# Performance work log

Measured on AMD Instinct MI355X. Metric: run time of the kernel, lower is better.

## Reference

```python
import jax, jax.numpy as jnp
import numpy as np

EMBED_DIM = 1024
NUM_HEADS = 16
HEAD_DIM = EMBED_DIM // NUM_HEADS


def setup_inputs() -> dict:
    key = jax.random.key(0)
    ks = jax.random.split(key, 9)
    B, S, D = 4, 2048, EMBED_DIM
    s = 1.0 / np.sqrt(D)
    return {
        "x": jax.random.normal(ks[0], (B, S, D), dtype=jnp.float32),
        "Wq": jax.random.normal(ks[1], (D, D), dtype=jnp.float32) * s,
        "bq": jnp.zeros((D,), dtype=jnp.float32),
        "Wk": jax.random.normal(ks[2], (D, D), dtype=jnp.float32) * s,
        "bk": jnp.zeros((D,), dtype=jnp.float32),
        "Wv": jax.random.normal(ks[3], (D, D), dtype=jnp.float32) * s,
        "bv": jnp.zeros((D,), dtype=jnp.float32),
        "Wo": jax.random.normal(ks[4], (D, D), dtype=jnp.float32) * s,
        "bo": jnp.zeros((D,), dtype=jnp.float32),
    }


def reference(x, Wq, bq, Wk, bk, Wv, bv, Wo, bo):
    B, S, D = x.shape
    H, Hd = NUM_HEADS, HEAD_DIM

    def proj(W, b):
        # [B,S,D] -> [B,H,S,Hd]
        y = jnp.einsum('bsd,de->bse', x, W) + b
        return y.reshape(B, S, H, Hd).transpose(0, 2, 1, 3)

    q = proj(Wq, bq)
    k = proj(Wk, bk)
    v = proj(Wv, bv)

    scale = 1.0 / jnp.sqrt(jnp.asarray(Hd, dtype=x.dtype))
    scores = jnp.einsum('bhqd,bhkd->bhqk', q, k) * scale  # [B,H,S,S]
    attn = jax.nn.softmax(scores, axis=-1)
    # dropout is identity in eval/inference mode
    heads = jnp.einsum('bhqk,bhkd->bhqd', attn, v)  # [B,H,S,Hd]
    heads = heads.transpose(0, 2, 1, 3).reshape(B, S, D)
    z = jnp.einsum('bsd,de->bse', heads, Wo) + bo
    return z
```

## Files before the change

### kernel.cpp

```cpp
#include <hip/hip_runtime.h>


typedef __attribute__((ext_vector_type(8))) short bf16x8;
typedef __attribute__((ext_vector_type(4))) float f32x4;
typedef __attribute__((ext_vector_type(4))) unsigned int u32x4;

#define MFMA16 __builtin_amdgcn_mfma_f32_16x16x32_bf16

__device__ __forceinline__ unsigned short f2bf(float f) {
  unsigned int u = __float_as_uint(f);
  u += 0x7fff + ((u >> 16) & 1);
  return (unsigned short)(u >> 16);
}

__device__ __forceinline__ unsigned int pkbf(float lo, float hi) {
  unsigned int a = __float_as_uint(lo) + 0x8000u;
  unsigned int b = __float_as_uint(hi) + 0x8000u;
  return __builtin_amdgcn_perm(b, a, 0x07060302u);
}

__device__ __forceinline__ bf16x8 pack4(unsigned int a, unsigned int b,
                                        unsigned int c, unsigned int d) {
  union { u32x4 u; bf16x8 v; } t;
  t.u = (u32x4){a, b, c, d};
  return t.v;
}

__device__ __forceinline__ void gl2l16(const unsigned short* g, unsigned short* l) {
  __builtin_amdgcn_global_load_lds((const __attribute__((address_space(1))) void*)g,
                                   (__attribute__((address_space(3))) void*)l, 16, 0, 0);
}
__device__ __forceinline__ void gl2l4(const unsigned short* g, unsigned short* l) {
  __builtin_amdgcn_global_load_lds((const __attribute__((address_space(1))) void*)g,
                                   (__attribute__((address_space(3))) void*)l, 4, 0, 0);
}

__global__ __launch_bounds__(256) void k_prep(const float* __restrict__ x,
                                              unsigned short* __restrict__ xb,
                                              const float* w0, const float* w1,
                                              const float* w2, const float* w3,
                                              unsigned short* o0, unsigned short* o1,
                                              unsigned short* o2, unsigned short* o3) {
  const int bid = blockIdx.x, tid = threadIdx.x;
  if (bid < 8192) {
    int i = (bid * 256 + tid) * 4;
    float4 v = *(const float4*)(x + i);
    ushort4 u;
    u.x = f2bf(v.x); u.y = f2bf(v.y); u.z = f2bf(v.z); u.w = f2bf(v.w);
    *(ushort4*)(xb + i) = u;
  } else {
    __shared__ float t[32][33];
    int tt = bid - 8192;
    int z = tt >> 10, rem = tt & 1023;
    const float* W = z == 0 ? w0 : z == 1 ? w1 : z == 2 ? w2 : w3;
    unsigned short* O = z == 0 ? o0 : z == 1 ? o1 : z == 2 ? o2 : o3;
    int e0 = (rem & 31) * 32, d0 = (rem >> 5) * 32;
    int tx = tid & 31, ty = tid >> 5;
    #pragma unroll
    for (int i = 0; i < 4; i++)
      t[ty + i * 8][tx] = W[(d0 + ty + i * 8) * 1024 + e0 + tx];
    __syncthreads();
    #pragma unroll
    for (int i = 0; i < 4; i++)
      O[(e0 + ty + i * 8) * 1024 + d0 + tx] = f2bf(t[tx][ty + i * 8]);
  }
}

__device__ __forceinline__ void kloop64(const unsigned short* __restrict__ gA,
                                        const unsigned short* __restrict__ gB,
                                        unsigned short* As, unsigned short* Bs,
                                        int w, int fm, int quad, int wr, int wc,
                                        f32x4 (&acc)[4][4]) {
  const int fsw = fm & 7;
  const int cs0 = (quad ^ fsw) * 8;
  const int cs1 = ((quad + 4) ^ fsw) * 8;
  unsigned short* lA = As + w * 2048;
  unsigned short* lB = Bs + w * 2048;

  for (int kb = 0; kb < 1024; kb += 64) {
    __syncthreads();
    #pragma unroll
    for (int i = 0; i < 4; i++) {
      gl2l16(gA + kb + i * 8192, lA + i * 512);
      gl2l16(gB + kb + i * 8192, lB + i * 512);
    }
    __syncthreads();
    #pragma unroll
    for (int kh = 0; kh < 2; kh++) {
      const int cs = kh ? cs1 : cs0;
      bf16x8 af[4], bfr[4];
      #pragma unroll
      for (int mt = 0; mt < 4; mt++)
        af[mt] = *(const bf16x8*)&As[(wr + mt * 16 + fm) * 64 + cs];
      #pragma unroll
      for (int nt = 0; nt < 4; nt++)
        bfr[nt] = *(const bf16x8*)&Bs[(wc + nt * 16 + fm) * 64 + cs];
      #pragma unroll
      for (int mt = 0; mt < 4; mt++)
        #pragma unroll
        for (int nt = 0; nt < 4; nt++)
          acc[mt][nt] = MFMA16(af[mt], bfr[nt], acc[mt][nt], 0, 0, 0);
    }
  }
}

__global__ __launch_bounds__(256) void gemm_qkv(const unsigned short* __restrict__ A,
                                                const unsigned short* __restrict__ Wt,
                                                const float* __restrict__ biq,
                                                const float* __restrict__ bik,
                                                const float* __restrict__ biv,
                                                unsigned short* __restrict__ oq,
                                                unsigned short* __restrict__ ok,
                                                unsigned short* __restrict__ ov,
                                                float qscale) {
  const int bid = blockIdx.x;
  const int xcd = bid & 7, c = bid >> 3;
  const int by = c & 63;
  const int phase = c >> 6;
  const int bx = xcd + phase * 8;
  const int bm0 = by * 128;
  const int bn0g = bx * 128;
  const int z = phase, bn0 = bn0g & 1023;

  const float* bias = z == 0 ? biq : z == 1 ? bik : biv;
  unsigned short* out = z == 0 ? oq : z == 1 ? ok : ov;
  const float scale = z == 0 ? qscale : 1.0f;

  const int tid = threadIdx.x;
  const int lane = tid & 63, w = tid >> 6;
  const int wr = (w >> 1) * 64, wc = (w & 1) * 64;
  const int fm = lane & 15, quad = lane >> 4;

  __shared__ unsigned short As[128 * 64];
  __shared__ unsigned short Bs[128 * 64];

  f32x4 acc[4][4] = {};

  const int srow = lane >> 3;
  const int sswz = ((lane & 7) ^ srow) * 8;
  const unsigned short* gA = A + (size_t)(bm0 + w * 32 + srow) * 1024 + sswz;
  const unsigned short* gB = Wt + (size_t)(bn0g + w * 32 + srow) * 1024 + sswz;

  kloop64(gA, gB, As, Bs, w, fm, quad, wr, wc, acc);

  float bv[4];
  #pragma unroll
  for (int nt = 0; nt < 4; nt++) bv[nt] = bias[bn0 + wc + nt * 16 + fm];

  #pragma unroll
  for (int mt = 0; mt < 4; mt++) {
    #pragma unroll
    for (int nt = 0; nt < 4; nt++) {
      #pragma unroll
      for (int r = 0; r < 4; r++) {
        int row = bm0 + wr + mt * 16 + quad * 4 + r;
        int col = bn0 + wc + nt * 16 + fm;
        float v = (acc[mt][nt][r] + bv[nt]) * scale;
        int b = row >> 11, s = row & 2047, h = col >> 6, hd = col & 63;
        if (z < 2)
          out[(((b << 4) + h) * 2048 + s) * 64 + hd] = f2bf(v);
        else
          out[(((b << 4) + h) * 64 + hd) * 2048 + s] = f2bf(v);
      }
    }
  }
}

__global__ __launch_bounds__(256) void gemm_out(const unsigned short* __restrict__ A,
                                                const unsigned short* __restrict__ Bt,
                                                const float* __restrict__ bias,
                                                float* __restrict__ out) {
  const int bid = blockIdx.x;
  const int xcd = bid & 7, c = bid >> 3;
  const int by = xcd * 8 + (c >> 3);
  const int bx = c & 7;
  const int bm0 = by * 128, bn0 = bx * 128;

  const int tid = threadIdx.x;
  const int lane = tid & 63, w = tid >> 6;
  const int wr = (w >> 1) * 64, wc = (w & 1) * 64;
  const int fm = lane & 15, quad = lane >> 4;

  __shared__ unsigned short As[128 * 64];
  __shared__ unsigned short Bs[128 * 64];

  f32x4 acc[4][4] = {};

  const int srow = lane >> 3;
  const int sswz = ((lane & 7) ^ srow) * 8;
  const unsigned short* gA = A + (size_t)(bm0 + w * 32 + srow) * 1024 + sswz;
  const unsigned short* gB = Bt + (size_t)(bn0 + w * 32 + srow) * 1024 + sswz;

  kloop64(gA, gB, As, Bs, w, fm, quad, wr, wc, acc);

  float bv[4];
  #pragma unroll
  for (int nt = 0; nt < 4; nt++) bv[nt] = bias[bn0 + wc + nt * 16 + fm];

  #pragma unroll
  for (int mt = 0; mt < 4; mt++)
    #pragma unroll
    for (int nt = 0; nt < 4; nt++)
      #pragma unroll
      for (int r = 0; r < 4; r++) {
        int row = bm0 + wr + mt * 16 + quad * 4 + r;
        int col = bn0 + wc + nt * 16 + fm;
        out[(size_t)row * 1024 + col] = acc[mt][nt][r] + bv[nt];
      }
}

__global__ __launch_bounds__(256, 4) void k_attn(const unsigned short* __restrict__ q,
                                                 const unsigned short* __restrict__ k,
                                                 const unsigned short* __restrict__ vt,
                                                 unsigned short* __restrict__ heads) {
  const int tid = threadIdx.x, lane = tid & 63, w = tid >> 6;
  const int fm = lane & 15, quad = lane >> 4, k0 = quad * 8;
  const int bh = blockIdx.x, qt = blockIdx.y;
  const int b = bh >> 4, h = bh & 15;
  const unsigned short* qg = q + (size_t)bh * 2048 * 64;
  const unsigned short* kg = k + (size_t)bh * 2048 * 64;
  const unsigned short* vg = vt + (size_t)bh * 64 * 2048;

  __shared__ unsigned short Ks[2 * 64 * 64];
  __shared__ unsigned short Vs[2 * 64 * 64];

  const int sr = lane >> 3;
  const int sswz = ((lane & 7) ^ sr) * 8;
  const unsigned short* gK = kg + (w * 16 + sr) * 64 + sswz;
  unsigned short* lK = Ks + w * 1024;
  unsigned short* lV = Vs + w * 1024;

  const unsigned short* gVp[8];
  {
    const int rhalf = lane >> 5;
    const int cpos = (lane & 31) >> 2;
    const int jlo = (lane & 1) * 2;
    const int jhi = ((lane >> 1) & 1) * 16;
    #pragma unroll
    for (int i = 0; i < 8; i++) {
      int rr = 2 * i + rhalf;
      int cc = cpos ^ (rr & 7);
      int koff = (cc & 4) * 8 + (cc & 3) * 4 + jlo + jhi;
      gVp[i] = vg + (size_t)(w * 16 + rr) * 2048 + koff;
    }
  }

  bf16x8 aq[2][2];
  #pragma unroll
  for (int mt = 0; mt < 2; mt++)
    #pragma unroll
    for (int kh = 0; kh < 2; kh++)
      aq[mt][kh] = *(const bf16x8*)&qg[(qt * 128 + w * 32 + mt * 16 + fm) * 64 + kh * 32 + k0];

  bf16x8 onesf;
  #pragma unroll
  for (int i = 0; i < 8; i++) onesf[i] = (short)0x3F80;

  f32x4 o[2][4] = {};
  f32x4 la[2] = {};
  const f32x4 zf = {0.f, 0.f, 0.f, 0.f};
  const int fsw = fm & 7;

  gl2l16(gK, lK);
  gl2l16(gK + 512, lK + 512);
  #pragma unroll
  for (int i = 0; i < 8; i++) gl2l4(gVp[i], lV + i * 128);
  __syncthreads();

  for (int kb = 0; kb < 32; kb++) {
    const int cur = kb & 1;
    if (kb < 31) {
      const int nb = cur ^ 1;
      gl2l16(gK + (kb + 1) * 4096,       lK + nb * 4096);
      gl2l16(gK + (kb + 1) * 4096 + 512, lK + nb * 4096 + 512);
      #pragma unroll
      for (int i = 0; i < 8; i++)
        gl2l4(gVp[i] + (kb + 1) * 64, lV + nb * 4096 + i * 128);
    }
    const unsigned short* Kb = Ks + cur * 4096;
    const unsigned short* Vb = Vs + cur * 4096;

    unsigned int pw[2][8];
    #pragma unroll
    for (int nt = 0; nt < 4; nt++) {
      bf16x8 bK0 = *(const bf16x8*)&Kb[(nt * 16 + fm) * 64 + ((quad ^ fsw) * 8)];
      f32x4 s0 = MFMA16(bK0, aq[0][0], zf, 0, 0, 0);
      f32x4 s1 = MFMA16(bK0, aq[1][0], zf, 0, 0, 0);
      bf16x8 bK1 = *(const bf16x8*)&Kb[(nt * 16 + fm) * 64 + (((4 + quad) ^ fsw) * 8)];
      s0 = MFMA16(bK1, aq[0][1], s0, 0, 0, 0);
      s1 = MFMA16(bK1, aq[1][1], s1, 0, 0, 0);
      pw[0][nt * 2 + 0] = pkbf(__builtin_amdgcn_exp2f(s0[0]), __builtin_amdgcn_exp2f(s0[1]));
      pw[0][nt * 2 + 1] = pkbf(__builtin_amdgcn_exp2f(s0[2]), __builtin_amdgcn_exp2f(s0[3]));
      pw[1][nt * 2 + 0] = pkbf(__builtin_amdgcn_exp2f(s1[0]), __builtin_amdgcn_exp2f(s1[1]));
      pw[1][nt * 2 + 1] = pkbf(__builtin_amdgcn_exp2f(s1[2]), __builtin_amdgcn_exp2f(s1[3]));
    }

    bf16x8 ap0k0 = pack4(pw[0][0], pw[0][1], pw[0][2], pw[0][3]);
    bf16x8 ap0k1 = pack4(pw[0][4], pw[0][5], pw[0][6], pw[0][7]);
    bf16x8 ap1k0 = pack4(pw[1][0], pw[1][1], pw[1][2], pw[1][3]);
    bf16x8 ap1k1 = pack4(pw[1][4], pw[1][5], pw[1][6], pw[1][7]);

    #pragma unroll
    for (int ks = 0; ks < 2; ks++) {
      bf16x8 a0 = ks ? ap0k1 : ap0k0;
      bf16x8 a1 = ks ? ap1k1 : ap1k0;
      la[0] = MFMA16(a0, onesf, la[0], 0, 0, 0);
      la[1] = MFMA16(a1, onesf, la[1], 0, 0, 0);
      #pragma unroll
      for (int ntO = 0; ntO < 4; ntO++) {
        bf16x8 bV = *(const bf16x8*)&Vb[(ntO * 16 + fm) * 64 + (((ks * 4 + quad) ^ fsw) * 8)];
        o[0][ntO] = MFMA16(a0, bV, o[0][ntO], 0, 0, 0);
        o[1][ntO] = MFMA16(a1, bV, o[1][ntO], 0, 0, 0);
      }
    }
    __syncthreads();
  }

  #pragma unroll
  for (int mt = 0; mt < 2; mt++)
    #pragma unroll
    for (int r = 0; r < 4; r++) {
      float inv = 1.0f / la[mt][r];
      int srw = qt * 128 + w * 32 + mt * 16 + quad * 4 + r;
      #pragma unroll
      for (int nt = 0; nt < 4; nt++)
        heads[(size_t)(b * 2048 + srw) * 1024 + h * 64 + nt * 16 + fm] =
            f2bf(o[mt][nt][r] * inv);
    }
}

extern "C" void kernel_launch(void* const* d_in, const int* in_sizes, int n_in,
                              void* d_out, int out_size, void* d_ws, size_t ws_size,
                              hipStream_t stream) {
  const float* x  = (const float*)d_in[0];
  const float* Wq = (const float*)d_in[1];
  const float* bq = (const float*)d_in[2];
  const float* Wk = (const float*)d_in[3];
  const float* bk = (const float*)d_in[4];
  const float* Wv = (const float*)d_in[5];
  const float* bv = (const float*)d_in[6];
  const float* Wo = (const float*)d_in[7];
  const float* bo = (const float*)d_in[8];
  float* out = (float*)d_out;

  char* ws = (char*)d_ws;
  unsigned short* xb  = (unsigned short*)(ws);
  unsigned short* wtq = (unsigned short*)(ws + (16u << 20));
  unsigned short* wtk = (unsigned short*)(ws + (18u << 20));
  unsigned short* wtv = (unsigned short*)(ws + (20u << 20));
  unsigned short* wto = (unsigned short*)(ws + (22u << 20));
  unsigned short* qb  = (unsigned short*)(ws + (24u << 20));
  unsigned short* kb2 = (unsigned short*)(ws + (40u << 20));
  unsigned short* vtb = (unsigned short*)(ws + (56u << 20));
  unsigned short* hb  = (unsigned short*)(ws + (72u << 20));

  k_prep<<<12288, 256, 0, stream>>>(x, xb, Wq, Wk, Wv, Wo, wtq, wtk, wtv, wto);

  const float qscale = 0.125f * 1.44269504088896f;
  gemm_qkv<<<1536, 256, 0, stream>>>(xb, wtq, bq, bk, bv, qb, kb2, vtb, qscale);

  k_attn<<<dim3(64, 16), 256, 0, stream>>>(qb, kb2, vtb, hb);

  gemm_out<<<512, 256, 0, stream>>>(hb, wto, bo, out);
}
```

Baseline: 281.9 us.

## Use 256x256 double-buffered pipelined GEMM tiles with 512 threads for projections

Result: slower. 313.1 us (+11.1%).

```diff
diff --git a/kernel.cpp b/kernel.cpp
--- a/kernel.cpp
+++ b/kernel.cpp
@@ -66,61 +66,99 @@
   }
 }
 
-__device__ __forceinline__ void kloop64(const unsigned short* __restrict__ gA,
-                                        const unsigned short* __restrict__ gB,
-                                        unsigned short* As, unsigned short* Bs,
-                                        int w, int fm, int quad, int wr, int wc,
-                                        f32x4 (&acc)[4][4]) {
+__device__ __forceinline__ void kloop256(const unsigned short* __restrict__ gA,
+                                         const unsigned short* __restrict__ gB,
+                                         unsigned short* As, unsigned short* Bs,
+                                         int w, int fm, int quad,
+                                         f32x4 (&acc)[8][4]) {
   const int fsw = fm & 7;
-  const int cs0 = (quad ^ fsw) * 8;
-  const int cs1 = ((quad + 4) ^ fsw) * 8;
-  unsigned short* lA = As + w * 2048;
-  unsigned short* lB = Bs + w * 2048;
-
-  for (int kb = 0; kb < 1024; kb += 64) {
-    __syncthreads();
-    #pragma unroll
-    for (int i = 0; i < 4; i++) {
-      gl2l16(gA + kb + i * 8192, lA + i * 512);
-      gl2l16(gB + kb + i * 8192, lB + i * 512);
-    }
-    __syncthreads();
-    #pragma unroll
-    for (int kh = 0; kh < 2; kh++) {
-      const int cs = kh ? cs1 : cs0;
-      bf16x8 af[4], bfr[4];
-      #pragma unroll
-      for (int mt = 0; mt < 4; mt++)
-        af[mt] = *(const bf16x8*)&As[(wr + mt * 16 + fm) * 64 + cs];
-      #pragma unroll
-      for (int nt = 0; nt < 4; nt++)
-        bfr[nt] = *(const bf16x8*)&Bs[(wc + nt * 16 + fm) * 64 + cs];
-      #pragma unroll
-      for (int mt = 0; mt < 4; mt++)
+  const int wm128 = (w >> 2) * 128;
+  const int wn64 = (w & 3) * 64;
+  const int c0 = (quad ^ fsw) * 8;
+  const int c1 = ((4 + quad) ^ fsw) * 8;
+
+#define STA(t, j) gl2l16(gA + (t) * 64 + (j) * 8192, As + ((t) & 1) * 16384 + w * 2048 + (j) * 512)
+#define STB(t, j) gl2l16(gB + (t) * 64 + (j) * 8192, Bs + ((t) & 1) * 16384 + w * 2048 + (j) * 512)
+
+  #pragma unroll
+  for (int j = 0; j < 4; ++j) STA(0, j);
+  #pragma unroll
+  for (int j = 0; j < 4; ++j) STB(0, j);
+  #pragma unroll
+  for (int j = 0; j < 4; ++j) STB(1, j);
+  asm volatile("s_waitcnt vmcnt(4)" ::: "memory");
+  asm volatile("s_barrier" ::: "memory");
+
+  for (int i = 0; i < 8; ++i) {
+    const int t0 = 2 * i, t1 = 2 * i + 1;
+    #pragma unroll
+    for (int par = 0; par < 2; ++par) {
+      const unsigned short* Ap = As + par * 16384;
+      const unsigned short* Bp = Bs + par * 16384;
+      bf16x8 bq[4][2];
+      #pragma unroll
+      for (int nt = 0; nt < 4; ++nt) {
+        const int br = (wn64 + nt * 16 + fm) * 64;
+        bq[nt][0] = *(const bf16x8*)&Bp[br + c0];
+        bq[nt][1] = *(const bf16x8*)&Bp[br + c1];
+      }
+      #pragma unroll
+      for (int q = 0; q < 4; ++q) {
+        const int r0 = (wm128 + (2 * q) * 16 + fm) * 64;
+        const int r1 = (wm128 + (2 * q + 1) * 16 + fm) * 64;
+        bf16x8 a0k0 = *(const bf16x8*)&Ap[r0 + c0];
+        bf16x8 a0k1 = *(const bf16x8*)&Ap[r0 + c1];
+        bf16x8 a1k0 = *(const bf16x8*)&Ap[r1 + c0];
+        bf16x8 a1k1 = *(const bf16x8*)&Ap[r1 + c1];
+        if (par == 0) {
+          if (q == 0)      { STA(t1, 0); STA(t1, 1); }
+          else if (q == 1) { STA(t1, 2); STA(t1, 3); }
+          else if (q == 2) { if (i < 7) { STB(t0 + 2, 0); STB(t0 + 2, 1); } }
+          else             { if (i < 7) { STB(t0 + 2, 2); STB(t0 + 2, 3); } }
+        } else {
+          if (q == 0)      { if (i < 7) { STA(t0 + 2, 0); STA(t0 + 2, 1); } }
+          else if (q == 1) { if (i < 7) { STA(t0 + 2, 2); STA(t0 + 2, 3); } }
+          else if (q == 2) { if (i < 7) { STB(t1 + 2, 0); STB(t1 + 2, 1); } }
+          else             { if (i < 7) { STB(t1 + 2, 2); STB(t1 + 2, 3); } }
+        }
+        asm volatile("s_barrier" ::: "memory");
+        __builtin_amdgcn_s_setprio(1);
         #pragma unroll
-        for (int nt = 0; nt < 4; nt++)
-          acc[mt][nt] = MFMA16(af[mt], bfr[nt], acc[mt][nt], 0, 0, 0);
+        for (int nt = 0; nt < 4; ++nt) {
+          acc[2 * q][nt]     = MFMA16(a0k0, bq[nt][0], acc[2 * q][nt], 0, 0, 0);
+          acc[2 * q][nt]     = MFMA16(a0k1, bq[nt][1], acc[2 * q][nt], 0, 0, 0);
+          acc[2 * q + 1][nt] = MFMA16(a1k0, bq[nt][0], acc[2 * q + 1][nt], 0, 0, 0);
+          acc[2 * q + 1][nt] = MFMA16(a1k1, bq[nt][1], acc[2 * q + 1][nt], 0, 0, 0);
+        }
+        __builtin_amdgcn_s_setprio(0);
+        if (par == 0 && q == 3) {
+          if (i < 7) asm volatile("s_waitcnt vmcnt(4)" ::: "memory");
+          else       asm volatile("s_waitcnt vmcnt(0)" ::: "memory");
+        }
+        if (par == 1 && q == 3)
+          asm volatile("s_waitcnt vmcnt(4)" ::: "memory");
+        asm volatile("s_barrier" ::: "memory");
+      }
     }
   }
-}
-
-__global__ __launch_bounds__(256) void gemm_qkv(const unsigned short* __restrict__ A,
-                                                const unsigned short* __restrict__ Wt,
-                                                const float* __restrict__ biq,
-                                                const float* __restrict__ bik,
-                                                const float* __restrict__ biv,
-                                                unsigned short* __restrict__ oq,
-                                                unsigned short* __restrict__ ok,
-                                                unsigned short* __restrict__ ov,
-                                                float qscale) {
+#undef STA
+#undef STB
+}
+
+__global__ __launch_bounds__(512, 2) void gemm_qkv(const unsigned short* __restrict__ A,
+                                                   const unsigned short* __restrict__ Wt,
+                                                   const float* __restrict__ biq,
+                                                   const float* __restrict__ bik,
+                                                   const float* __restrict__ biv,
+                                                   unsigned short* __restrict__ oq,
+                                                   unsigned short* __restrict__ ok,
+                                                   unsigned short* __restrict__ ov,
+                                                   float qscale) {
   const int bid = blockIdx.x;
-  const int xcd = bid & 7, c = bid >> 3;
-  const int by = c & 63;
-  const int phase = c >> 6;
-  const int bx = xcd + phase * 8;
-  const int bm0 = by * 128;
-  const int bn0g = bx * 128;
-  const int z = phase, bn0 = bn0g & 1023;
+  const int bx = bid % 12, by = bid / 12;
+  const int bm0 = by * 256;
+  const int bn0g = bx * 256;
+  const int z = bn0g >> 10, bn0 = bn0g & 1023;
 
   const float* bias = z == 0 ? biq : z == 1 ? bik : biv;
   unsigned short* out = z == 0 ? oq : z == 1 ? ok : ov;
@@ -128,33 +166,33 @@
 
   const int tid = threadIdx.x;
   const int lane = tid & 63, w = tid >> 6;
-  const int wr = (w >> 1) * 64, wc = (w & 1) * 64;
   const int fm = lane & 15, quad = lane >> 4;
-
-  __shared__ unsigned short As[128 * 64];
-  __shared__ unsigned short Bs[128 * 64];
-
-  f32x4 acc[4][4] = {};
+  const int wm128 = (w >> 2) * 128, wn64 = (w & 3) * 64;
+
+  __shared__ unsigned short As[2 * 256 * 64];
+  __shared__ unsigned short Bs[2 * 256 * 64];
+
+  f32x4 acc[8][4] = {};
 
   const int srow = lane >> 3;
   const int sswz = ((lane & 7) ^ srow) * 8;
   const unsigned short* gA = A + (size_t)(bm0 + w * 32 + srow) * 1024 + sswz;
   const unsigned short* gB = Wt + (size_t)(bn0g + w * 32 + srow) * 1024 + sswz;
 
-  kloop64(gA, gB, As, Bs, w, fm, quad, wr, wc, acc);
+  kloop256(gA, gB, As, Bs, w, fm, quad, acc);
 
   float bv[4];
   #pragma unroll
-  for (int nt = 0; nt < 4; nt++) bv[nt] = bias[bn0 + wc + nt * 16 + fm];
-
-  #pragma unroll
-  for (int mt = 0; mt < 4; mt++) {
+  for (int nt = 0; nt < 4; nt++) bv[nt] = bias[bn0 + wn64 + nt * 16 + fm];
+
+  #pragma unroll
+  for (int mt = 0; mt < 8; mt++) {
     #pragma unroll
     for (int nt = 0; nt < 4; nt++) {
       #pragma unroll
       for (int r = 0; r < 4; r++) {
-        int row = bm0 + wr + mt * 16 + quad * 4 + r;
-        int col = bn0 + wc + nt * 16 + fm;
+        int row = bm0 + wm128 + mt * 16 + quad * 4 + r;
+        int col = bn0 + wn64 + nt * 16 + fm;
         float v = (acc[mt][nt][r] + bv[nt]) * scale;
         int b = row >> 11, s = row & 2047, h = col >> 6, hd = col & 63;
         if (z < 2)
@@ -166,45 +204,43 @@
   }
 }
 
-__global__ __launch_bounds__(256) void gemm_out(const unsigned short* __restrict__ A,
-                                                const unsigned short* __restrict__ Bt,
-                                                const float* __restrict__ bias,
-                                                float* __restrict__ out) {
+__global__ __launch_bounds__(512, 2) void gemm_out(const unsigned short* __restrict__ A,
+                                                   const unsigned short* __restrict__ Bt,
+                                                   const float* __restrict__ bias,
+                                                   float* __restrict__ out) {
   const int bid = blockIdx.x;
-  const int xcd = bid & 7, c = bid >> 3;
-  const int by = xcd * 8 + (c >> 3);
-  const int bx = c & 7;
-  const int bm0 = by * 128, bn0 = bx * 128;
+  const int bx = bid & 3, by = bid >> 2;
+  const int bm0 = by * 256, bn0 = bx * 256;
 
   const int tid = threadIdx.x;
   const int lane = tid & 63, w = tid >> 6;
-  const int wr = (w >> 1) * 64, wc = (w & 1) * 64;
   const int fm = lane & 15, quad = lane >> 4;
-
-  __shared__ unsigned short As[128 * 64];
-  __shared__ unsigned short Bs[128 * 64];
-
-  f32x4 acc[4][4] = {};
+  const int wm128 = (w >> 2) * 128, wn64 = (w & 3) * 64;
+
+  __shared__ unsigned short As[2 * 256 * 64];
+  __shared__ unsigned short Bs[2 * 256 * 64];
+
+  f32x4 acc[8][4] = {};
 
   const int srow = lane >> 3;
   const int sswz = ((lane & 7) ^ srow) * 8;
   const unsigned short* gA = A + (size_t)(bm0 + w * 32 + srow) * 1024 + sswz;
   const unsigned short* gB = Bt + (size_t)(bn0 + w * 32 + srow) * 1024 + sswz;
 
-  kloop64(gA, gB, As, Bs, w, fm, quad, wr, wc, acc);
+  kloop256(gA, gB, As, Bs, w, fm, quad, acc);
 
   float bv[4];
   #pragma unroll
-  for (int nt = 0; nt < 4; nt++) bv[nt] = bias[bn0 + wc + nt * 16 + fm];
-
-  #pragma unroll
-  for (int mt = 0; mt < 4; mt++)
+  for (int nt = 0; nt < 4; nt++) bv[nt] = bias[bn0 + wn64 + nt * 16 + fm];
+
+  #pragma unroll
+  for (int mt = 0; mt < 8; mt++)
     #pragma unroll
     for (int nt = 0; nt < 4; nt++)
       #pragma unroll
       for (int r = 0; r < 4; r++) {
-        int row = bm0 + wr + mt * 16 + quad * 4 + r;
-        int col = bn0 + wc + nt * 16 + fm;
+        int row = bm0 + wm128 + mt * 16 + quad * 4 + r;
+        int col = bn0 + wn64 + nt * 16 + fm;
         out[(size_t)row * 1024 + col] = acc[mt][nt][r] + bv[nt];
       }
 }
@@ -357,9 +393,9 @@
   k_prep<<<12288, 256, 0, stream>>>(x, xb, Wq, Wk, Wv, Wo, wtq, wtk, wtv, wto);
 
   const float qscale = 0.125f * 1.44269504088896f;
-  gemm_qkv<<<1536, 256, 0, stream>>>(xb, wtq, bq, bk, bv, qb, kb2, vtb, qscale);
+  gemm_qkv<<<384, 512, 0, stream>>>(xb, wtq, bq, bk, bv, qb, kb2, vtb, qscale);
 
   k_attn<<<dim3(64, 16), 256, 0, stream>>>(qb, kb2, vtb, hb);
 
-  gemm_out<<<512, 256, 0, stream>>>(hb, wto, bo, out);
-}
+  gemm_out<<<128, 512, 0, stream>>>(hb, wto, bo, out);
+}
```
